# Kernel tuning notes

Hardware: AMD Instinct MI355X
Metric: run time of the kernel (lower is better)

The kernel has to match this reference:

```python
import jax, jax.numpy as jnp
import numpy as np

GROUP = 64  # hardcoded group_size in the module


def setup_inputs() -> dict:
    key = jax.random.key(0)
    ks = jax.random.split(key, 7)
    B, S, K, N, R = 64, 1, 4096, 12288, 32
    G = K // GROUP
    x = jax.random.normal(ks[0], (B, S, K), jnp.float32)
    # int4 weight residual values in [-8, 7]
    q_w = jax.random.randint(ks[1], (N, K), -8, 8, jnp.int32)
    # per-(group, out_channel) positive scales, shape [G, N] as in the module buffer
    wscales = jax.random.uniform(ks[2], (G, N), jnp.float32, 1e-3, 2e-2)
    lora_down = jax.random.normal(ks[3], (K, R), jnp.float32) * 0.02
    lora_up = jax.random.normal(ks[4], (N, R), jnp.float32) * 0.02
    smooth = jax.random.uniform(ks[5], (K,), jnp.float32, 0.5, 2.0)
    bias = jax.random.normal(ks[6], (N,), jnp.float32) * 0.01
    return {"x": x, "q_w": q_w, "wscales": wscales, "lora_down": lora_down,
            "lora_up": lora_up, "smooth": smooth, "bias": bias}


def reference(x, q_w, wscales, lora_down, lora_up, smooth, bias):
    # x: [B, S, K]; q_w: [N, K] int4 values; wscales: [K//64, N]
    B, S, K = x.shape
    G = K // GROUP
    # smoothing divide (per in-channel)
    x_div = x / smooth  # [B, S, K]
    # --- activation W4A4 path: symmetric int4 per-token per-group quantization ---
    xg = x_div.reshape(B, S, G, GROUP)
    ascale = jnp.maximum(jnp.max(jnp.abs(xg), axis=-1) / 7.0, 1e-8)  # [B, S, G]
    xq = jnp.clip(jnp.round(xg / ascale[..., None]), -8.0, 7.0)
    x_deq = (xq * ascale[..., None]).reshape(B, S, K)  # dequantized activation
    # --- dequantize int4 weight residual: w[n,k] = q[n,k] * wscales[k//64, n] ---
    w_deq = q_w.astype(jnp.float32) * jnp.repeat(wscales, GROUP, axis=0).T  # [N, K]
    # main quantized GEMM
    y = jnp.einsum('bsk,nk->bsn', x_deq, w_deq)  # [B, S, N]
    # low-rank SVD branch on the full-precision smoothed activation
    y = y + (x_div @ lora_down) @ lora_up.T
    y = y + bias
    return y
```

## Files before the change

kernel.cpp:

```cpp
#include <hip/hip_runtime.h>
#include <hip/hip_bf16.h>

#define K_DIM 4096
#define N_DIM 12288
#define B_DIM 64
#define G_DIM 64
#define R_DIM 32
#define NT_DIM 768

typedef int v4i __attribute__((ext_vector_type(4)));

__device__ __forceinline__ int pack4(const v4i a) {
    return (a.x & 255) | ((a.y & 255) << 8) | ((a.z & 255) << 16) | (a.w << 24);
}

__global__ __launch_bounds__(256) void quant_packed_kernel(
    const float* __restrict__ x, const float* __restrict__ smooth,
    char* __restrict__ xq_p, float* __restrict__ ascale) {
    const int b = blockIdx.x >> 4;
    const int gq = blockIdx.x & 15;
    const int w = threadIdx.x >> 6, lane = threadIdx.x & 63;
    const int g = gq * 4 + w;
    const int k = g * 64 + lane;
    const float xd = x[b * K_DIM + k] / smooth[k];
    float a = fabsf(xd);
    #pragma unroll
    for (int off = 32; off; off >>= 1) a = fmaxf(a, __shfl_xor(a, off));
    const float as = fmaxf(a / 7.0f, 1e-8f);
    float q = rintf(xd / as);
    q = fminf(fmaxf(q, -8.0f), 7.0f);
    const int bt = b >> 4, b15 = b & 15;
    const int quad = lane >> 4, kin = lane & 15;
    xq_p[((((size_t)bt * G_DIM + g) * 64) + quad * 16 + b15) * 16 + kin] = (char)(int)q;
    if (lane == 0) ascale[b * G_DIM + g] = as;
}

__global__ __launch_bounds__(256) void lora_down_kernel(
    const float* __restrict__ x, const float* __restrict__ smooth,
    const float* __restrict__ ld, float* __restrict__ t) {
    const int b = blockIdx.x >> 4;
    const int kc = blockIdx.x & 15;
    const int r = threadIdx.x & 31;
    const int c = threadIdx.x >> 5;
    const int k0 = kc * 256 + c * 32;
    float acc = 0.f;
    #pragma unroll 8
    for (int k = k0; k < k0 + 32; ++k) {
        const float xd = x[b * K_DIM + k] / smooth[k];
        acc += xd * ld[k * R_DIM + r];
    }
    __shared__ float red[256];
    red[threadIdx.x] = acc;
    __syncthreads();
    if (threadIdx.x < 32) {
        float s = 0.f;
        #pragma unroll
        for (int c2 = 0; c2 < 8; ++c2) s += red[c2 * 32 + threadIdx.x];
        atomicAdd(&t[b * R_DIM + threadIdx.x], s);
    }
}

__global__ __launch_bounds__(256) void main_fused_kernel(
    const int* __restrict__ qw, const float* __restrict__ wscales,
    const v4i* __restrict__ xq_p, const float* __restrict__ ascale,
    const float* __restrict__ t, const float* __restrict__ lora_up,
    const float* __restrict__ bias, float* __restrict__ out) {
    __shared__ float s_ws[G_DIM * 16];
    __shared__ float s_as[G_DIM * 68];
    __shared__ float s_t[B_DIM * R_DIM];
    __shared__ int   s_qp[2][1088];

    const int nt = blockIdx.x;
    const int n0 = nt * 16;
    const int tid = threadIdx.x;

    const int srow = tid >> 4;
    const int scol = tid & 15;
    const int* gptr = qw + (size_t)(n0 + srow) * K_DIM + scol * 4;

    for (int i = tid; i < G_DIM * 16; i += 256)
        s_ws[i] = wscales[(i >> 4) * N_DIM + n0 + (i & 15)];
    for (int i = tid; i < B_DIM * G_DIM; i += 256) {
        const int b = i >> 6, g = i & 63;
        s_as[g * 68 + b] = ascale[i];
    }
    for (int i = tid; i < B_DIM * R_DIM; i += 256) s_t[i] = t[i];

    {
        v4i qa[4];
        #pragma unroll
        for (int i = 0; i < 4; ++i) qa[i] = *(const v4i*)(gptr + i * 64);
        #pragma unroll
        for (int i = 0; i < 4; ++i)
            s_qp[0][srow * 68 + i * 16 + scol] = pack4(qa[i]);
    }
    __syncthreads();

    const int w = tid >> 6, lane = tid & 63;
    const int col = lane & 15, quad = lane >> 4;

    float facc[4] = {0.f, 0.f, 0.f, 0.f};
    const v4i zero = {0, 0, 0, 0};
    const v4i* xbase = xq_p + (size_t)w * G_DIM * 64 + lane;
    const char* rdbase0 = (const char*)&s_qp[0][0] + col * 272 + quad * 16;
    const char* rdbase1 = (const char*)&s_qp[1][0] + col * 272 + quad * 16;

    #pragma unroll 2
    for (int j = 0; j < 16; ++j) {
        v4i qa[4];
        if (j < 15) {
            const int* p = gptr + (j + 1) * 256;
            #pragma unroll
            for (int i = 0; i < 4; ++i) qa[i] = *(const v4i*)(p + i * 64);
        }
        const char* rd = (j & 1) ? rdbase1 : rdbase0;
        #pragma unroll
        for (int gi = 0; gi < 4; ++gi) {
            const int g = j * 4 + gi;
            const v4i bq = *(const v4i*)(rd + gi * 64);
            const v4i xa = xbase[(size_t)g * 64];
            const v4i d = __builtin_amdgcn_mfma_i32_16x16x64_i8(xa, bq, zero, 0, 0, 0);
            const float wsc = s_ws[g * 16 + col];
            const float4 as4 = *(const float4*)&s_as[g * 68 + w * 16 + quad * 4];
            facc[0] = fmaf(as4.x * wsc, (float)d[0], facc[0]);
            facc[1] = fmaf(as4.y * wsc, (float)d[1], facc[1]);
            facc[2] = fmaf(as4.z * wsc, (float)d[2], facc[2]);
            facc[3] = fmaf(as4.w * wsc, (float)d[3], facc[3]);
        }
        if (j < 15) {
            int* wb = (j & 1) ? &s_qp[0][0] : &s_qp[1][0];
            #pragma unroll
            for (int i = 0; i < 4; ++i)
                wb[srow * 68 + i * 16 + scol] = pack4(qa[i]);
        }
        __syncthreads();
    }

    const int n = n0 + col;
    float4 lu[8];
    {
        const float4* lp = (const float4*)(lora_up + (size_t)n * R_DIM);
        #pragma unroll
        for (int i = 0; i < 8; ++i) lu[i] = lp[i];
    }
    const float bs = bias[n];
    #pragma unroll
    for (int r = 0; r < 4; ++r) {
        const int b = w * 16 + quad * 4 + r;
        float acc = facc[r] + bs;
        #pragma unroll
        for (int r2 = 0; r2 < 8; ++r2) {
            const float4 tv = *(const float4*)&s_t[b * R_DIM + r2 * 4];
            acc += tv.x * lu[r2].x + tv.y * lu[r2].y +
                   tv.z * lu[r2].z + tv.w * lu[r2].w;
        }
        out[(size_t)b * N_DIM + n] = acc;
    }
}

extern "C" void kernel_launch(void* const* d_in, const int* in_sizes, int n_in,
                              void* d_out, int out_size, void* d_ws, size_t ws_size,
                              hipStream_t stream) {
    const float* x         = (const float*)d_in[0];
    const int*   q_w       = (const int*)d_in[1];
    const float* wscales   = (const float*)d_in[2];
    const float* lora_down = (const float*)d_in[3];
    const float* lora_up   = (const float*)d_in[4];
    const float* smooth    = (const float*)d_in[5];
    const float* bias      = (const float*)d_in[6];
    float* out = (float*)d_out;

    char*  xq     = (char*)d_ws;
    float* ascale = (float*)((char*)d_ws + 262144);
    float* t      = (float*)((char*)d_ws + 262144 + 16384);

    hipMemsetAsync(t, 0, B_DIM * R_DIM * sizeof(float), stream);
    quant_packed_kernel<<<B_DIM * 16, 256, 0, stream>>>(x, smooth, xq, ascale);
    lora_down_kernel<<<B_DIM * 16, 256, 0, stream>>>(x, smooth, lora_down, t);
    main_fused_kernel<<<NT_DIM, 256, 0, stream>>>(q_w, wscales, (const v4i*)xq,
                                                  ascale, t, lora_up, bias, out);
}
```

Before: 299.7 us.

## Fuse quant and lora-down kernels, drop memset, double weight chunk per stage

Merges the activation quantization and LoRA-down projection into one kernel that shares the smoothed activations through shared memory. The atomic accumulation and memset are replaced by per-chunk partial sums, which the main kernel reduces when it loads them. The main GEMM loop now stages 8 groups per iteration instead of 4, using a new padded LDS layout, and is fully unrolled. This removes two launches and halves the number of barriers, at the cost of more LDS, more registers, and 16 redundant partial-sum reads per block.

```diff
diff --git a/kernel.cpp b/kernel.cpp
--- a/kernel.cpp
+++ b/kernel.cpp
@@ -14,61 +14,60 @@
     return (a.x & 255) | ((a.y & 255) << 8) | ((a.z & 255) << 16) | (a.w << 24);
 }
 
-__global__ __launch_bounds__(256) void quant_packed_kernel(
+__global__ __launch_bounds__(256) void quant_lora_kernel(
     const float* __restrict__ x, const float* __restrict__ smooth,
-    char* __restrict__ xq_p, float* __restrict__ ascale) {
+    const float* __restrict__ ld, char* __restrict__ xq_p,
+    float* __restrict__ ascale, float* __restrict__ t_part) {
     const int b = blockIdx.x >> 4;
-    const int gq = blockIdx.x & 15;
-    const int w = threadIdx.x >> 6, lane = threadIdx.x & 63;
-    const int g = gq * 4 + w;
-    const int k = g * 64 + lane;
+    const int kc = blockIdx.x & 15;
+    const int tid = threadIdx.x;
+    const int k = kc * 256 + tid;
+
+    __shared__ float sx[256];
+    __shared__ float red[256];
+
     const float xd = x[b * K_DIM + k] / smooth[k];
+    sx[tid] = xd;
+
+    const int lane = tid & 63;
     float a = fabsf(xd);
     #pragma unroll
     for (int off = 32; off; off >>= 1) a = fmaxf(a, __shfl_xor(a, off));
     const float as = fmaxf(a / 7.0f, 1e-8f);
     float q = rintf(xd / as);
     q = fminf(fmaxf(q, -8.0f), 7.0f);
+    const int g = kc * 4 + (tid >> 6);
     const int bt = b >> 4, b15 = b & 15;
     const int quad = lane >> 4, kin = lane & 15;
     xq_p[((((size_t)bt * G_DIM + g) * 64) + quad * 16 + b15) * 16 + kin] = (char)(int)q;
     if (lane == 0) ascale[b * G_DIM + g] = as;
-}
+    __syncthreads();
 
-__global__ __launch_bounds__(256) void lora_down_kernel(
-    const float* __restrict__ x, const float* __restrict__ smooth,
-    const float* __restrict__ ld, float* __restrict__ t) {
-    const int b = blockIdx.x >> 4;
-    const int kc = blockIdx.x & 15;
-    const int r = threadIdx.x & 31;
-    const int c = threadIdx.x >> 5;
-    const int k0 = kc * 256 + c * 32;
+    const int r = tid & 31, c = tid >> 5;
+    const int kb = kc * 256 + c * 32;
     float acc = 0.f;
     #pragma unroll 8
-    for (int k = k0; k < k0 + 32; ++k) {
-        const float xd = x[b * K_DIM + k] / smooth[k];
-        acc += xd * ld[k * R_DIM + r];
-    }
-    __shared__ float red[256];
-    red[threadIdx.x] = acc;
+    for (int kk = 0; kk < 32; ++kk)
+        acc += sx[c * 32 + kk] * ld[(size_t)(kb + kk) * R_DIM + r];
+    red[tid] = acc;
     __syncthreads();
-    if (threadIdx.x < 32) {
+    if (tid < 32) {
         float s = 0.f;
         #pragma unroll
-        for (int c2 = 0; c2 < 8; ++c2) s += red[c2 * 32 + threadIdx.x];
-        atomicAdd(&t[b * R_DIM + threadIdx.x], s);
+        for (int c2 = 0; c2 < 8; ++c2) s += red[c2 * 32 + tid];
+        t_part[kc * (B_DIM * R_DIM) + b * R_DIM + tid] = s;
     }
 }
 
 __global__ __launch_bounds__(256) void main_fused_kernel(
     const int* __restrict__ qw, const float* __restrict__ wscales,
     const v4i* __restrict__ xq_p, const float* __restrict__ ascale,
-    const float* __restrict__ t, const float* __restrict__ lora_up,
+    const float* __restrict__ t_part, const float* __restrict__ lora_up,
     const float* __restrict__ bias, float* __restrict__ out) {
     __shared__ float s_ws[G_DIM * 16];
     __shared__ float s_as[G_DIM * 68];
     __shared__ float s_t[B_DIM * R_DIM];
-    __shared__ int   s_qp[2][1088];
+    __shared__ int   s_qp[2][2560];
 
     const int nt = blockIdx.x;
     const int n0 = nt * 16;
@@ -77,6 +76,7 @@
     const int srow = tid >> 4;
     const int scol = tid & 15;
     const int* gptr = qw + (size_t)(n0 + srow) * K_DIM + scol * 4;
+    const int lds_w = srow * 20 + scol;
 
     for (int i = tid; i < G_DIM * 16; i += 256)
         s_ws[i] = wscales[(i >> 4) * N_DIM + n0 + (i & 15)];
@@ -84,15 +84,19 @@
         const int b = i >> 6, g = i & 63;
         s_as[g * 68 + b] = ascale[i];
     }
-    for (int i = tid; i < B_DIM * R_DIM; i += 256) s_t[i] = t[i];
+    for (int i = tid; i < B_DIM * R_DIM; i += 256) {
+        float s = 0.f;
+        #pragma unroll
+        for (int kc = 0; kc < 16; ++kc) s += t_part[kc * (B_DIM * R_DIM) + i];
+        s_t[i] = s;
+    }
 
     {
-        v4i qa[4];
+        v4i qa[8];
         #pragma unroll
-        for (int i = 0; i < 4; ++i) qa[i] = *(const v4i*)(gptr + i * 64);
+        for (int i = 0; i < 8; ++i) qa[i] = *(const v4i*)(gptr + i * 64);
         #pragma unroll
-        for (int i = 0; i < 4; ++i)
-            s_qp[0][srow * 68 + i * 16 + scol] = pack4(qa[i]);
+        for (int i = 0; i < 8; ++i) s_qp[0][i * 320 + lds_w] = pack4(qa[i]);
     }
     __syncthreads();
 
@@ -102,22 +106,22 @@
     float facc[4] = {0.f, 0.f, 0.f, 0.f};
     const v4i zero = {0, 0, 0, 0};
     const v4i* xbase = xq_p + (size_t)w * G_DIM * 64 + lane;
-    const char* rdbase0 = (const char*)&s_qp[0][0] + col * 272 + quad * 16;
-    const char* rdbase1 = (const char*)&s_qp[1][0] + col * 272 + quad * 16;
+    const char* rdb0 = (const char*)&s_qp[0][0] + col * 80 + quad * 16;
+    const char* rdb1 = (const char*)&s_qp[1][0] + col * 80 + quad * 16;
 
-    #pragma unroll 2
-    for (int j = 0; j < 16; ++j) {
-        v4i qa[4];
-        if (j < 15) {
-            const int* p = gptr + (j + 1) * 256;
+    #pragma unroll
+    for (int j = 0; j < 8; ++j) {
+        v4i qa[8];
+        if (j < 7) {
+            const int* p = gptr + (j + 1) * 512;
             #pragma unroll
-            for (int i = 0; i < 4; ++i) qa[i] = *(const v4i*)(p + i * 64);
+            for (int i = 0; i < 8; ++i) qa[i] = *(const v4i*)(p + i * 64);
         }
-        const char* rd = (j & 1) ? rdbase1 : rdbase0;
+        const char* rd = (j & 1) ? rdb1 : rdb0;
         #pragma unroll
-        for (int gi = 0; gi < 4; ++gi) {
-            const int g = j * 4 + gi;
-            const v4i bq = *(const v4i*)(rd + gi * 64);
+        for (int gi = 0; gi < 8; ++gi) {
+            const int g = j * 8 + gi;
+            const v4i bq = *(const v4i*)(rd + gi * 1280);
             const v4i xa = xbase[(size_t)g * 64];
             const v4i d = __builtin_amdgcn_mfma_i32_16x16x64_i8(xa, bq, zero, 0, 0, 0);
             const float wsc = s_ws[g * 16 + col];
@@ -127,11 +131,10 @@
             facc[2] = fmaf(as4.z * wsc, (float)d[2], facc[2]);
             facc[3] = fmaf(as4.w * wsc, (float)d[3], facc[3]);
         }
-        if (j < 15) {
+        if (j < 7) {
             int* wb = (j & 1) ? &s_qp[0][0] : &s_qp[1][0];
             #pragma unroll
-            for (int i = 0; i < 4; ++i)
-                wb[srow * 68 + i * 16 + scol] = pack4(qa[i]);
+            for (int i = 0; i < 8; ++i) wb[i * 320 + lds_w] = pack4(qa[i]);
         }
         __syncthreads();
     }
@@ -172,11 +175,10 @@
 
     char*  xq     = (char*)d_ws;
     float* ascale = (float*)((char*)d_ws + 262144);
-    float* t      = (float*)((char*)d_ws + 262144 + 16384);
+    float* t_part = (float*)((char*)d_ws + 262144 + 16384);
 
-    hipMemsetAsync(t, 0, B_DIM * R_DIM * sizeof(float), stream);
-    quant_packed_kernel<<<B_DIM * 16, 256, 0, stream>>>(x, smooth, xq, ascale);
-    lora_down_kernel<<<B_DIM * 16, 256, 0, stream>>>(x, smooth, lora_down, t);
+    quant_lora_kernel<<<B_DIM * 16, 256, 0, stream>>>(x, smooth, lora_down,
+                                                      xq, ascale, t_part);
     main_fused_kernel<<<NT_DIM, 256, 0, stream>>>(q_w, wscales, (const v4i*)xq,
-                                                  ascale, t, lora_up, bias, out);
+                                                  ascale, t_part, lora_up, bias, out);
 }
```

New measurement: 391.7 us. +30.7%, slower.
